# Performance work log

Measured on AMD Instinct MI355X. Metric: run time of the kernel, lower is better.

Reference implementation:

```python
import jax, jax.numpy as jnp
import numpy as np

EPS = 1e-4

def mp_normalize(x, axis):
    # normalize() from the source: divisor = eps + ||x|| * sqrt(n_norm_elems / n_elems)
    # alpha = sqrt(norm.numel()/x.numel()) = 1/sqrt(prod of reduced dims)
    red = int(np.prod([x.shape[a] for a in axis])) if isinstance(axis, (list, tuple)) else x.shape[axis]
    w = jnp.sqrt(jnp.sum(jnp.square(x.astype(jnp.float32)), axis=axis, keepdims=True))
    w = EPS + w / np.sqrt(red)
    return x / w.astype(x.dtype)

def mp_linear(x, w, gain):
    # MP_Conv with (1,1) kernel == per-token linear; w: [out, in]
    fan_in = w.shape[1]
    wn = mp_normalize(w.astype(jnp.float32), axis=(1,)) * (gain / np.sqrt(fan_in))
    return jnp.einsum('bse,oe->bso', x, wn.astype(x.dtype))

def attention(query, gain, w_q, w_k, w_v, w_o, num_heads=16, attn_balance=0.5):
    B, S, E = query.shape
    hd = E // num_heads
    res = query
    q = mp_linear(query, w_q, gain).reshape(B, S, num_heads, hd).transpose(0, 2, 1, 3)  # bnsh
    k = mp_linear(query, w_k, gain).reshape(B, S, num_heads, hd).transpose(0, 2, 1, 3)
    v = mp_linear(query, w_v, gain).reshape(B, S, num_heads, hd).transpose(0, 2, 1, 3)
    q = mp_normalize(q, axis=(3,))
    k = mp_normalize(k, axis=(3,))
    # NOTE: contracts over sequence axis -> [B, H, hd, hd] (faithful to source einsum)
    scores = jnp.einsum('bnsh,bnsk->bnhk', q, k / np.sqrt(S))
    attn = jax.nn.softmax(scores, axis=3)
    o = jnp.einsum('bnhk,bnsk->bnsh', attn, v)  # [B, H, S, hd]
    o = o.transpose(0, 2, 1, 3).reshape(B, S, E)
    out = mp_linear(o, w_o, gain)
    t = attn_balance
    return (res * (1.0 - t) + out * t) / np.sqrt((1 - t) ** 2 + t ** 2)

def setup_inputs() -> dict:
    key = jax.random.key(0)
    ks = jax.random.split(key, 5)
    B, S, E = 4, 4096, 1024
    return {
        'query': jax.random.normal(ks[0], (B, S, E), dtype=jnp.float32),
        'gain': jnp.float32(1.0),
        'w_q': jax.random.normal(ks[1], (E, E), dtype=jnp.float32),
        'w_k': jax.random.normal(ks[2], (E, E), dtype=jnp.float32),
        'w_v': jax.random.normal(ks[3], (E, E), dtype=jnp.float32),
        'w_o': jax.random.normal(ks[4], (E, E), dtype=jnp.float32),
    }

def reference(query, gain, w_q, w_k, w_v, w_o):
    return attention(query, gain, w_q, w_k, w_v, w_o)
```

## Files before the change

### kernel.cpp

```cpp
#include <hip/hip_runtime.h>
#include <math.h>


typedef __bf16 bf16;
typedef __bf16 bf16x8 __attribute__((ext_vector_type(8)));
typedef __bf16 bf16x4 __attribute__((ext_vector_type(4)));
typedef float  f32x4  __attribute__((ext_vector_type(4)));

#define DEVINL __device__ __forceinline__

DEVINL void gload_lds16(const void* g, void* l) {
  __builtin_amdgcn_global_load_lds(
      (__attribute__((address_space(1))) void*)(void*)g,
      (__attribute__((address_space(3))) void*)l, 16, 0, 0);
}

static constexpr int Sq = 4096;
static constexpr int Ek = 1024;
static constexpr int Mrows = 16384;

__global__ __launch_bounds__(256) void k_prep_w(
    const float* __restrict__ wq, const float* __restrict__ wk,
    const float* __restrict__ wv, const float* __restrict__ wo,
    const float* __restrict__ gain_p,
    bf16* __restrict__ WN, bf16* __restrict__ WNO) {
  int r = blockIdx.x;
  int mat = r >> 10, row = r & 1023;
  const float* w = (mat == 0) ? wq : (mat == 1) ? wk : (mat == 2) ? wv : wo;
  int t = threadIdx.x;
  f32x4 v = *(const f32x4*)&w[(size_t)row * 1024 + t * 4];
  float ss = v[0]*v[0] + v[1]*v[1] + v[2]*v[2] + v[3]*v[3];
#pragma unroll
  for (int m2 = 1; m2 < 64; m2 <<= 1) ss += __shfl_xor(ss, m2);
  __shared__ float red[4];
  if ((t & 63) == 0) red[t >> 6] = ss;
  __syncthreads();
  float tot = red[0] + red[1] + red[2] + red[3];
  float g = gain_p[0];
  float scale = (g * 0.03125f) / (1e-4f + sqrtf(tot) * 0.03125f);
  bf16x4 ov;
  ov[0] = (bf16)(v[0]*scale); ov[1] = (bf16)(v[1]*scale);
  ov[2] = (bf16)(v[2]*scale); ov[3] = (bf16)(v[3]*scale);
  if (mat < 3) *(bf16x4*)&WN [(size_t)r   * 1024 + t * 4] = ov;
  else         *(bf16x4*)&WNO[(size_t)row * 1024 + t * 4] = ov;
}

__global__ __launch_bounds__(256) void k_cvt_x(const float* __restrict__ x,
                                               bf16* __restrict__ xb) {
  size_t idx = (size_t)blockIdx.x * 256 + threadIdx.x;
  const size_t n8 = (size_t)Mrows * Ek / 8;
  for (size_t i = idx; i < n8; i += (size_t)2048 * 256) {
    f32x4 a = *(const f32x4*)&x[i * 8];
    f32x4 b = *(const f32x4*)&x[i * 8 + 4];
    bf16x8 ov;
    ov[0]=(bf16)a[0]; ov[1]=(bf16)a[1]; ov[2]=(bf16)a[2]; ov[3]=(bf16)a[3];
    ov[4]=(bf16)b[0]; ov[5]=(bf16)b[1]; ov[6]=(bf16)b[2]; ov[7]=(bf16)b[3];
    *(bf16x8*)&xb[i * 8] = ov;
  }
}


DEVINL bf16x8 lds_frag(const bf16* base, int row, int kelem) {
  int byte = row * 128 + kelem * 2;
  byte ^= (row & 7) << 4;
  return *(const bf16x8*)((const char*)base + byte);
}

#define PH_BAR() do { __builtin_amdgcn_s_barrier();                    \
    asm volatile("s_waitcnt lgkmcnt(0)" ::: "memory");                 \
    __builtin_amdgcn_sched_barrier(0);                                 \
    __builtin_amdgcn_s_setprio(1); } while (0)
#define PH_END() do { __builtin_amdgcn_s_setprio(0);                   \
    __builtin_amdgcn_s_barrier(); } while (0)

template <int EPI>
__global__ __launch_bounds__(512, 2) void k_gemm256(
    const bf16* __restrict__ A, const bf16* __restrict__ Bw,
    void* __restrict__ Cout, const float* __restrict__ resid,
    int N, int NXB) {
  constexpr int K = 1024;
  constexpr int NT = K / 64;
  __shared__ bf16 lds[2][2][256 * 64];

  int nwg = gridDim.x;
  int bid = blockIdx.x;
  int cpx = nwg >> 3;
  int swz = (bid & 7) * cpx + (bid >> 3);
  int by = swz / NXB, bx = swz % NXB;
  int m0 = by * 256, n0 = bx * 256;

  int t = threadIdx.x;
  int lane = t & 63, w = t >> 6;
  int wr = w >> 2, wc = w & 3;
  int fr = lane & 15;
  int kof = (lane >> 4) * 8;

  int srow = t >> 3;
  int sslot = (t & 7) ^ (srow & 7);
  const bf16* ag = A  + (size_t)(m0 + srow) * K + sslot * 8;
  const bf16* bg = Bw + (size_t)(n0 + srow) * K + sslot * 8;

  f32x4 acc[8][4] = {};

  int cur = 0;
  {
    bf16* An = &lds[0][0][0];
    bf16* Bn = &lds[0][1][0];
#pragma unroll
    for (int q = 0; q < 4; ++q)
      gload_lds16(ag + (size_t)q * 64 * K, &An[q * 4096 + t * 8]);
#pragma unroll
    for (int q = 0; q < 4; ++q)
      gload_lds16(bg + (size_t)q * 64 * K, &Bn[q * 4096 + t * 8]);
    asm volatile("s_waitcnt vmcnt(0)" ::: "memory");
    __builtin_amdgcn_s_barrier();
  }

  for (int kt = 0; kt < NT; ++kt) {
    const bf16* Ac = &lds[cur][0][0];
    const bf16* Bc = &lds[cur][1][0];
    bf16* An = &lds[cur ^ 1][0][0];
    bf16* Bn = &lds[cur ^ 1][1][0];
    bool pf = (kt + 1 < NT);
    int knext = (kt + 1) * 64;

    bf16x8 afr[4], bfr[4];

#pragma unroll
    for (int i = 0; i < 4; ++i) bfr[i] = lds_frag(Bc, wc * 64 + i * 16 + fr, kof);
#pragma unroll
    for (int i = 0; i < 4; ++i) afr[i] = lds_frag(Ac, wr * 128 + i * 16 + fr, kof);
    if (pf) {
#pragma unroll
      for (int q = 0; q < 4; ++q)
        gload_lds16(ag + (size_t)q * 64 * K + knext, &An[q * 4096 + t * 8]);
    }
    PH_BAR();
#pragma unroll
    for (int mi = 0; mi < 4; ++mi)
#pragma unroll
      for (int ni = 0; ni < 4; ++ni)
        acc[mi][ni] = __builtin_amdgcn_mfma_f32_16x16x32_bf16(afr[mi], bfr[ni], acc[mi][ni], 0, 0, 0);
    PH_END();

#pragma unroll
    for (int i = 0; i < 4; ++i) afr[i] = lds_frag(Ac, wr * 128 + (4 + i) * 16 + fr, kof);
    if (pf) {
#pragma unroll
      for (int q = 0; q < 4; ++q)
        gload_lds16(bg + (size_t)q * 64 * K + knext, &Bn[q * 4096 + t * 8]);
    }
    PH_BAR();
#pragma unroll
    for (int mi = 0; mi < 4; ++mi)
#pragma unroll
      for (int ni = 0; ni < 4; ++ni)
        acc[4 + mi][ni] = __builtin_amdgcn_mfma_f32_16x16x32_bf16(afr[mi], bfr[ni], acc[4 + mi][ni], 0, 0, 0);
    PH_END();

#pragma unroll
    for (int i = 0; i < 4; ++i) bfr[i] = lds_frag(Bc, wc * 64 + i * 16 + fr, 32 + kof);
#pragma unroll
    for (int i = 0; i < 4; ++i) afr[i] = lds_frag(Ac, wr * 128 + i * 16 + fr, 32 + kof);
    PH_BAR();
#pragma unroll
    for (int mi = 0; mi < 4; ++mi)
#pragma unroll
      for (int ni = 0; ni < 4; ++ni)
        acc[mi][ni] = __builtin_amdgcn_mfma_f32_16x16x32_bf16(afr[mi], bfr[ni], acc[mi][ni], 0, 0, 0);
    PH_END();

#pragma unroll
    for (int i = 0; i < 4; ++i) afr[i] = lds_frag(Ac, wr * 128 + (4 + i) * 16 + fr, 32 + kof);
    PH_BAR();
#pragma unroll
    for (int mi = 0; mi < 4; ++mi)
#pragma unroll
      for (int ni = 0; ni < 4; ++ni)
        acc[4 + mi][ni] = __builtin_amdgcn_mfma_f32_16x16x32_bf16(afr[mi], bfr[ni], acc[4 + mi][ni], 0, 0, 0);
    __builtin_amdgcn_s_setprio(0);
    asm volatile("s_waitcnt vmcnt(0)" ::: "memory");
    __builtin_amdgcn_s_barrier();
    cur ^= 1;
  }

  int colbase = n0 + wc * 64 + fr;
  if constexpr (EPI == 0) {
    bf16* C = (bf16*)Cout;
    bool dn = (n0 + wc * 64) < 2048;
#pragma unroll
    for (int mi = 0; mi < 8; ++mi) {
#pragma unroll
      for (int r = 0; r < 4; ++r) {
        float scale = 1.f;
        if (dn) {
          float ss = 0.f;
#pragma unroll
          for (int ni = 0; ni < 4; ++ni) { float v = acc[mi][ni][r]; ss += v * v; }
          ss += __shfl_xor(ss, 1); ss += __shfl_xor(ss, 2);
          ss += __shfl_xor(ss, 4); ss += __shfl_xor(ss, 8);
          scale = 1.f / (1e-4f + sqrtf(ss) * 0.125f);
        }
        int row = m0 + wr * 128 + mi * 16 + ((lane >> 4) << 2) + r;
        size_t base = (size_t)row * N + colbase;
#pragma unroll
        for (int ni = 0; ni < 4; ++ni)
          C[base + ni * 16] = (bf16)(acc[mi][ni][r] * scale);
      }
    }
  } else {
    float* C = (float*)Cout;
#pragma unroll
    for (int mi = 0; mi < 8; ++mi) {
#pragma unroll
      for (int r = 0; r < 4; ++r) {
        int row = m0 + wr * 128 + mi * 16 + ((lane >> 4) << 2) + r;
        size_t base = (size_t)row * N + colbase;
#pragma unroll
        for (int ni = 0; ni < 4; ++ni) {
          size_t idx = base + ni * 16;
          C[idx] = (resid[idx] + acc[mi][ni][r]) * 0.70710678118654752f;
        }
      }
    }
  }
}

__global__ __launch_bounds__(256) void k_scores(const bf16* __restrict__ qkv,
                                                float* __restrict__ part) {
  __shared__ float Qs[64][64];
  __shared__ float Ks[64][64];
  int blk = blockIdx.x;
  int p = blk >> 6, c = blk & 63;
  int b = p >> 4, n = p & 15;
  int t = threadIdx.x;
  int j = t & 7;
  size_t rowbase = ((size_t)(b * 4096 + c * 64)) * 3072 + n * 64 + j * 8;
#pragma unroll
  for (int i = 0; i < 2; ++i) {
    int sl = i * 32 + (t >> 3);
    bf16x8 qv = *(const bf16x8*)&qkv[rowbase + (size_t)sl * 3072];
    bf16x8 kv = *(const bf16x8*)&qkv[rowbase + (size_t)sl * 3072 + 1024];
    f32x4 q0, q1, k0v, k1v;
    q0[0]=(float)qv[0]; q0[1]=(float)qv[1]; q0[2]=(float)qv[2]; q0[3]=(float)qv[3];
    q1[0]=(float)qv[4]; q1[1]=(float)qv[5]; q1[2]=(float)qv[6]; q1[3]=(float)qv[7];
    k0v[0]=(float)kv[0]; k0v[1]=(float)kv[1]; k0v[2]=(float)kv[2]; k0v[3]=(float)kv[3];
    k1v[0]=(float)kv[4]; k1v[1]=(float)kv[5]; k1v[2]=(float)kv[6]; k1v[3]=(float)kv[7];
    *(f32x4*)&Qs[sl][j * 8]     = q0;
    *(f32x4*)&Qs[sl][j * 8 + 4] = q1;
    *(f32x4*)&Ks[sl][j * 8]     = k0v;
    *(f32x4*)&Ks[sl][j * 8 + 4] = k1v;
  }
  __syncthreads();
  int h0 = (t >> 4) << 2, k0 = (t & 15) << 2;
  float acc[4][4] = {};
  for (int s = 0; s < 64; ++s) {
    f32x4 q  = *(const f32x4*)&Qs[s][h0];
    f32x4 kk = *(const f32x4*)&Ks[s][k0];
#pragma unroll
    for (int a = 0; a < 4; ++a) {
      acc[a][0] += q[a] * kk[0]; acc[a][1] += q[a] * kk[1];
      acc[a][2] += q[a] * kk[2]; acc[a][3] += q[a] * kk[3];
    }
  }
  size_t base = (size_t)blk * 4096;
#pragma unroll
  for (int a = 0; a < 4; ++a) {
    f32x4 st; st[0]=acc[a][0]; st[1]=acc[a][1]; st[2]=acc[a][2]; st[3]=acc[a][3];
    *(f32x4*)&part[base + (size_t)(h0 + a) * 64 + k0] = st;
  }
}

__global__ __launch_bounds__(256) void k_softmax(const float* __restrict__ part,
                                                 bf16* __restrict__ attn) {
  int blk = blockIdx.x;
  int p = blk >> 2, q = blk & 3;
  int t = threadIdx.x;
  int e0 = q * 1024 + t * 4;
  const float* pp = part + (size_t)p * 64 * 4096 + e0;
  f32x4 s = {};
#pragma unroll 4
  for (int c = 0; c < 64; ++c) {
    f32x4 v = *(const f32x4*)&pp[(size_t)c * 4096];
    s[0] += v[0]; s[1] += v[1]; s[2] += v[2]; s[3] += v[3];
  }
  const float sc = 1.0f / 64.0f;
  s[0] *= sc; s[1] *= sc; s[2] *= sc; s[3] *= sc;
  float mx = fmaxf(fmaxf(s[0], s[1]), fmaxf(s[2], s[3]));
  mx = fmaxf(mx, __shfl_xor(mx, 1));
  mx = fmaxf(mx, __shfl_xor(mx, 2));
  mx = fmaxf(mx, __shfl_xor(mx, 4));
  mx = fmaxf(mx, __shfl_xor(mx, 8));
  f32x4 e;
  e[0] = __expf(s[0] - mx); e[1] = __expf(s[1] - mx);
  e[2] = __expf(s[2] - mx); e[3] = __expf(s[3] - mx);
  float sum = e[0] + e[1] + e[2] + e[3];
  sum += __shfl_xor(sum, 1);
  sum += __shfl_xor(sum, 2);
  sum += __shfl_xor(sum, 4);
  sum += __shfl_xor(sum, 8);
  float inv = 1.0f / sum;
  bf16x4 ov;
  ov[0] = (bf16)(e[0] * inv); ov[1] = (bf16)(e[1] * inv);
  ov[2] = (bf16)(e[2] * inv); ov[3] = (bf16)(e[3] * inv);
  *(bf16x4*)&attn[(size_t)p * 4096 + e0] = ov;
}

__global__ __launch_bounds__(256) void k_pv(const bf16* __restrict__ qkv,
                                            const bf16* __restrict__ attn,
                                            bf16* __restrict__ o) {
  int blk = blockIdx.x;
  int p = blk >> 4, ch = blk & 15;
  int b = p >> 4, n = p & 15;
  int t = threadIdx.x, lane = t & 63, w = t >> 6;
  int s0 = ch * 256 + w * 64;
  size_t vrow0 = (size_t)(b * 4096 + s0);
  const bf16* At = attn + (size_t)p * 4096;
  f32x4 acc[4][4] = {};
#pragma unroll
  for (int ks = 0; ks < 2; ++ks) {
    int kof = ks * 32 + ((lane >> 4) << 3);
    bf16x8 vf[4], af[4];
#pragma unroll
    for (int mi = 0; mi < 4; ++mi)
      vf[mi] = *(const bf16x8*)&qkv[(vrow0 + mi * 16 + (lane & 15)) * 3072 + 2048 + n * 64 + kof];
#pragma unroll
    for (int ni = 0; ni < 4; ++ni)
      af[ni] = *(const bf16x8*)&At[(size_t)(ni * 16 + (lane & 15)) * 64 + kof];
#pragma unroll
    for (int mi = 0; mi < 4; ++mi)
#pragma unroll
      for (int ni = 0; ni < 4; ++ni)
        acc[mi][ni] = __builtin_amdgcn_mfma_f32_16x16x32_bf16(vf[mi], af[ni], acc[mi][ni], 0, 0, 0);
  }
#pragma unroll
  for (int mi = 0; mi < 4; ++mi)
#pragma unroll
    for (int r = 0; r < 4; ++r) {
      int srow = s0 + mi * 16 + ((lane >> 4) << 2) + r;
      size_t base = ((size_t)(b * 4096 + srow)) * 1024 + n * 64 + (lane & 15);
#pragma unroll
      for (int ni = 0; ni < 4; ++ni)
        o[base + ni * 16] = (bf16)acc[mi][ni][r];
    }
}

extern "C" void kernel_launch(void* const* d_in, const int* in_sizes, int n_in,
                              void* d_out, int out_size, void* d_ws, size_t ws_size,
                              hipStream_t stream) {
  const float* x    = (const float*)d_in[0];
  const float* gain = (const float*)d_in[1];
  const float* wq   = (const float*)d_in[2];
  const float* wk   = (const float*)d_in[3];
  const float* wv   = (const float*)d_in[4];
  const float* wo   = (const float*)d_in[5];

  char* ws = (char*)d_ws;
  bf16*  WN   = (bf16*)(ws + 0);
  bf16*  WNO  = (bf16*)(ws + 6291456);
  bf16*  xb   = (bf16*)(ws + 8388608);
  bf16*  qkv  = (bf16*)(ws + 41943040);
  float* part = (float*)(ws + 142606336);
  bf16*  attn = (bf16*)(ws + 209715200);
  bf16*  o    = xb;

  k_prep_w<<<4096, 256, 0, stream>>>(wq, wk, wv, wo, gain, WN, WNO);
  k_cvt_x<<<2048, 256, 0, stream>>>(x, xb);
  k_gemm256<0><<<768, 512, 0, stream>>>(xb, WN, (void*)qkv, nullptr, 3072, 12);
  k_scores<<<4096, 256, 0, stream>>>(qkv, part);
  k_softmax<<<256, 256, 0, stream>>>(part, attn);
  k_pv<<<1024, 256, 0, stream>>>(qkv, attn, o);
  k_gemm256<1><<<256, 512, 0, stream>>>(o, WNO, d_out, x, 1024, 4);
}
```

Baseline: 357.6 us.

## Split GEMM K-tiles into half-tile LDS buffers with deeper prefetch pipeline

Splits each 64-wide K tile of A and B into two 32-wide half buffers, each double-buffered, with a new 64-byte-row swizzle. Global-to-LDS loads for the next half tile are issued one or two phases ahead. Partial vmcnt(8) waits replace the full vmcnt(0) drain at the end of every K iteration. The goal is to keep more memory traffic in flight and stop stalling on every load per iteration, at the cost of more complex vmcnt accounting that must exactly match the issue order.

```diff
diff --git a/kernel.cpp b/kernel.cpp
--- a/kernel.cpp
+++ b/kernel.cpp
@@ -15,7 +15,6 @@
       (__attribute__((address_space(3))) void*)l, 16, 0, 0);
 }
 
-static constexpr int Sq = 4096;
 static constexpr int Ek = 1024;
 static constexpr int Mrows = 16384;
 
@@ -59,10 +58,9 @@
   }
 }
 
-
-DEVINL bf16x8 lds_frag(const bf16* base, int row, int kelem) {
-  int byte = row * 128 + kelem * 2;
-  byte ^= (row & 7) << 4;
+DEVINL bf16x8 frag32(const bf16* base, int row, int kof8) {
+  int byte = row * 64 + kof8 * 2;
+  byte ^= (row & 3) << 4;
   return *(const bf16x8*)((const char*)base + byte);
 }
 
@@ -72,6 +70,9 @@
     __builtin_amdgcn_s_setprio(1); } while (0)
 #define PH_END() do { __builtin_amdgcn_s_setprio(0);                   \
     __builtin_amdgcn_s_barrier(); } while (0)
+#define PH_ENDW() do { __builtin_amdgcn_s_setprio(0);                  \
+    asm volatile("s_waitcnt vmcnt(8)" ::: "memory");                   \
+    __builtin_amdgcn_s_barrier(); } while (0)
 
 template <int EPI>
 __global__ __launch_bounds__(512, 2) void k_gemm256(
@@ -79,11 +80,13 @@
     void* __restrict__ Cout, const float* __restrict__ resid,
     int N, int NXB) {
   constexpr int K = 1024;
-  constexpr int NT = K / 64;
-  __shared__ bf16 lds[2][2][256 * 64];
-
-  int nwg = gridDim.x;
-  int bid = blockIdx.x;
+  constexpr int NT = 16;
+  __shared__ bf16 A0l[2][256 * 32];
+  __shared__ bf16 A1l[2][256 * 32];
+  __shared__ bf16 B0l[2][256 * 32];
+  __shared__ bf16 B1l[2][256 * 32];
+
+  int nwg = gridDim.x, bid = blockIdx.x;
   int cpx = nwg >> 3;
   int swz = (bid & 7) * cpx + (bid >> 3);
   int by = swz / NXB, bx = swz % NXB;
@@ -95,45 +98,47 @@
   int fr = lane & 15;
   int kof = (lane >> 4) * 8;
 
-  int srow = t >> 3;
-  int sslot = (t & 7) ^ (srow & 7);
-  const bf16* ag = A  + (size_t)(m0 + srow) * K + sslot * 8;
-  const bf16* bg = Bw + (size_t)(n0 + srow) * K + sslot * 8;
+  int srH = t >> 2;
+  int sgH = (t & 3) ^ (srH & 3);
+  const bf16* asrcH = A  + (size_t)(m0 + srH) * K + sgH * 8;
+  const bf16* bsrcH = Bw + (size_t)(n0 + srH) * K + sgH * 8;
+  const size_t RSTEP = (size_t)128 * K;
 
   f32x4 acc[8][4] = {};
 
-  int cur = 0;
-  {
-    bf16* An = &lds[0][0][0];
-    bf16* Bn = &lds[0][1][0];
-#pragma unroll
-    for (int q = 0; q < 4; ++q)
-      gload_lds16(ag + (size_t)q * 64 * K, &An[q * 4096 + t * 8]);
-#pragma unroll
-    for (int q = 0; q < 4; ++q)
-      gload_lds16(bg + (size_t)q * 64 * K, &Bn[q * 4096 + t * 8]);
-    asm volatile("s_waitcnt vmcnt(0)" ::: "memory");
-    __builtin_amdgcn_s_barrier();
-  }
+  gload_lds16(asrcH,               &A0l[0][t * 8]);
+  gload_lds16(asrcH + RSTEP,       &A0l[0][4096 + t * 8]);
+  gload_lds16(bsrcH,               &B0l[0][t * 8]);
+  gload_lds16(bsrcH + RSTEP,       &B0l[0][4096 + t * 8]);
+  gload_lds16(asrcH + 32,          &A1l[0][t * 8]);
+  gload_lds16(asrcH + 32 + RSTEP,  &A1l[0][4096 + t * 8]);
+  gload_lds16(bsrcH + 32,          &B1l[0][t * 8]);
+  gload_lds16(bsrcH + 32 + RSTEP,  &B1l[0][4096 + t * 8]);
+  gload_lds16(asrcH + 64,          &A0l[1][t * 8]);
+  gload_lds16(asrcH + 64 + RSTEP,  &A0l[1][4096 + t * 8]);
+  gload_lds16(bsrcH + 64,          &B0l[1][t * 8]);
+  gload_lds16(bsrcH + 64 + RSTEP,  &B0l[1][4096 + t * 8]);
+  asm volatile("s_waitcnt vmcnt(8)" ::: "memory");
+  __builtin_amdgcn_s_barrier();
 
   for (int kt = 0; kt < NT; ++kt) {
-    const bf16* Ac = &lds[cur][0][0];
-    const bf16* Bc = &lds[cur][1][0];
-    bf16* An = &lds[cur ^ 1][0][0];
-    bf16* Bn = &lds[cur ^ 1][1][0];
-    bool pf = (kt + 1 < NT);
-    int knext = (kt + 1) * 64;
+    int cur = kt & 1, nxt = cur ^ 1;
+    const bf16* A0c = A0l[cur];
+    const bf16* A1c = A1l[cur];
+    const bf16* B0c = B0l[cur];
+    const bf16* B1c = B1l[cur];
+    bool p1 = (kt + 1 < NT), p2 = (kt + 2 < NT);
+    int kn1 = (kt + 1) * 64, kn2 = (kt + 2) * 64;
 
     bf16x8 afr[4], bfr[4];
 
 #pragma unroll
-    for (int i = 0; i < 4; ++i) bfr[i] = lds_frag(Bc, wc * 64 + i * 16 + fr, kof);
-#pragma unroll
-    for (int i = 0; i < 4; ++i) afr[i] = lds_frag(Ac, wr * 128 + i * 16 + fr, kof);
-    if (pf) {
-#pragma unroll
-      for (int q = 0; q < 4; ++q)
-        gload_lds16(ag + (size_t)q * 64 * K + knext, &An[q * 4096 + t * 8]);
+    for (int i = 0; i < 4; ++i) bfr[i] = frag32(B0c, wc * 64 + i * 16 + fr, kof);
+#pragma unroll
+    for (int i = 0; i < 4; ++i) afr[i] = frag32(A0c, wr * 128 + i * 16 + fr, kof);
+    if (p1) {
+      gload_lds16(asrcH + kn1 + 32,         &A1l[nxt][t * 8]);
+      gload_lds16(asrcH + kn1 + 32 + RSTEP, &A1l[nxt][4096 + t * 8]);
     }
     PH_BAR();
 #pragma unroll
@@ -144,11 +149,10 @@
     PH_END();
 
 #pragma unroll
-    for (int i = 0; i < 4; ++i) afr[i] = lds_frag(Ac, wr * 128 + (4 + i) * 16 + fr, kof);
-    if (pf) {
-#pragma unroll
-      for (int q = 0; q < 4; ++q)
-        gload_lds16(bg + (size_t)q * 64 * K + knext, &Bn[q * 4096 + t * 8]);
+    for (int i = 0; i < 4; ++i) afr[i] = frag32(A0c, wr * 128 + (4 + i) * 16 + fr, kof);
+    if (p1) {
+      gload_lds16(bsrcH + kn1 + 32,         &B1l[nxt][t * 8]);
+      gload_lds16(bsrcH + kn1 + 32 + RSTEP, &B1l[nxt][4096 + t * 8]);
     }
     PH_BAR();
 #pragma unroll
@@ -156,12 +160,16 @@
 #pragma unroll
       for (int ni = 0; ni < 4; ++ni)
         acc[4 + mi][ni] = __builtin_amdgcn_mfma_f32_16x16x32_bf16(afr[mi], bfr[ni], acc[4 + mi][ni], 0, 0, 0);
-    PH_END();
-
-#pragma unroll
-    for (int i = 0; i < 4; ++i) bfr[i] = lds_frag(Bc, wc * 64 + i * 16 + fr, 32 + kof);
-#pragma unroll
-    for (int i = 0; i < 4; ++i) afr[i] = lds_frag(Ac, wr * 128 + i * 16 + fr, 32 + kof);
+    PH_ENDW();
+
+#pragma unroll
+    for (int i = 0; i < 4; ++i) bfr[i] = frag32(B1c, wc * 64 + i * 16 + fr, kof);
+#pragma unroll
+    for (int i = 0; i < 4; ++i) afr[i] = frag32(A1c, wr * 128 + i * 16 + fr, kof);
+    if (p2) {
+      gload_lds16(asrcH + kn2,              &A0l[cur][t * 8]);
+      gload_lds16(asrcH + kn2 + RSTEP,      &A0l[cur][4096 + t * 8]);
+    }
     PH_BAR();
 #pragma unroll
     for (int mi = 0; mi < 4; ++mi)
@@ -171,17 +179,18 @@
     PH_END();
 
 #pragma unroll
-    for (int i = 0; i < 4; ++i) afr[i] = lds_frag(Ac, wr * 128 + (4 + i) * 16 + fr, 32 + kof);
+    for (int i = 0; i < 4; ++i) afr[i] = frag32(A1c, wr * 128 + (4 + i) * 16 + fr, kof);
+    if (p2) {
+      gload_lds16(bsrcH + kn2,              &B0l[cur][t * 8]);
+      gload_lds16(bsrcH + kn2 + RSTEP,      &B0l[cur][4096 + t * 8]);
+    }
     PH_BAR();
 #pragma unroll
     for (int mi = 0; mi < 4; ++mi)
 #pragma unroll
       for (int ni = 0; ni < 4; ++ni)
         acc[4 + mi][ni] = __builtin_amdgcn_mfma_f32_16x16x32_bf16(afr[mi], bfr[ni], acc[4 + mi][ni], 0, 0, 0);
-    __builtin_amdgcn_s_setprio(0);
-    asm volatile("s_waitcnt vmcnt(0)" ::: "memory");
-    __builtin_amdgcn_s_barrier();
-    cur ^= 1;
+    PH_ENDW();
   }
 
   int colbase = n0 + wc * 64 + fr;
```

New measurement: 398.0 us. +11.3%, slower.
